# Optimization experiments

Hardware: AMD Instinct MI355X
Metric: run time of the kernel (lower is better)

## Reference

```python
import jax, jax.numpy as jnp
import numpy as np

B, GNN_DIM, TR_DIM, F = 16384, 512, 768, 1024


def setup_inputs() -> dict:
    key = jax.random.key(0)
    ks = jax.random.split(key, 16)
    s = 0.02
    return {
        "gnn_features": jax.random.normal(ks[0], (B, GNN_DIM), jnp.float32),
        "transformer_features": jax.random.normal(ks[1], (B, TR_DIM), jnp.float32),
        # gnn_projector / transformer_projector (torch Linear: y = x @ W.T + b)
        "Wg": jax.random.normal(ks[2], (F, GNN_DIM), jnp.float32) * s,
        "bg": jnp.zeros((F,), jnp.float32),
        "Wt": jax.random.normal(ks[3], (F, TR_DIM), jnp.float32) * s,
        "bt": jnp.zeros((F,), jnp.float32),
        # MultiheadAttention value-projection slice of in_proj_weight and out_proj.
        # With seq_len==1 the softmax over a single key is identically 1, so the
        # attention output is exactly out_proj(v_proj(key)); Q/K projections do
        # not affect the output (their gradients are exactly zero).
        "Wv": jax.random.normal(ks[4], (F, F), jnp.float32) * s,
        "bv": jnp.zeros((F,), jnp.float32),
        "Wo": jax.random.normal(ks[5], (F, F), jnp.float32) * s,
        "bo": jnp.zeros((F,), jnp.float32),
        # fusion_layers: Linear(2F -> F), GELU, Dropout(eval: identity), Linear(F -> F)
        "W1": jax.random.normal(ks[6], (F, 2 * F), jnp.float32) * s,
        "b1": jnp.zeros((F,), jnp.float32),
        "W2": jax.random.normal(ks[7], (F, F), jnp.float32) * s,
        "b2": jnp.zeros((F,), jnp.float32),
    }


def reference(gnn_features, transformer_features, Wg, bg, Wt, bt, Wv, bv, Wo, bo, W1, b1, W2, b2):
    # projections to fusion space  [B, F]
    gnn_proj = gnn_features @ Wg.T + bg
    tr_proj = transformer_features @ Wt.T + bt
    # degenerate single-token cross-attention: softmax over 1 key == 1, so
    # attn(q, k, v=k) = out_proj(v_proj(k)) regardless of the query.
    gnn_attended = (tr_proj @ Wv.T + bv) @ Wo.T + bo   # attention(gnn_seq, tr_seq, tr_seq)
    tr_attended = (gnn_proj @ Wv.T + bv) @ Wo.T + bo   # attention(tr_seq, gnn_seq, gnn_seq)
    combined = jnp.concatenate([gnn_attended, tr_attended], axis=-1)  # [B, 2F]
    h = jax.nn.gelu(combined @ W1.T + b1, approximate=False)          # exact GELU (torch default)
    fused = h @ W2.T + b2
    return fused + gnn_proj + tr_proj
```

## Files before the change

kernel.cpp:

```cpp
#include <hip/hip_runtime.h>
#include <cmath>

#define GAS __attribute__((address_space(1)))
#define LAS __attribute__((address_space(3)))

typedef __bf16 bf16x8 __attribute__((ext_vector_type(8)));
typedef float f32x4 __attribute__((ext_vector_type(4)));
typedef float f32x16 __attribute__((ext_vector_type(16)));

__device__ __forceinline__ void gload16(const void* g, void* l) {
    __builtin_amdgcn_global_load_lds((const GAS void*)g, (LAS void*)l, 16, 0, 0);
}

__global__ void k_prep(const float* __restrict__ gnn, const float* __restrict__ tr,
                       const float* __restrict__ Wo, const float* __restrict__ W1,
                       const float* __restrict__ W2, const float* __restrict__ Wg,
                       const float* __restrict__ Wt, const float* __restrict__ Wv,
                       const float* __restrict__ bv, const float* __restrict__ bo,
                       const float* __restrict__ bt, const float* __restrict__ bg,
                       __bf16* __restrict__ X, __bf16* __restrict__ W1ab,
                       __bf16* __restrict__ Wp, __bf16* __restrict__ Wv_b,
                       __bf16* __restrict__ WoT, __bf16* __restrict__ WgT,
                       __bf16* __restrict__ WtT,
                       float* __restrict__ b_att, float* __restrict__ vb_t,
                       float* __restrict__ vb_g) {
    __shared__ float t[32][33];
    int b = blockIdx.x;
    int tid = threadIdx.x;
    if (b < 12928) {
        const float* src; __bf16* dst; int sld, dld, base, c8;
        if (b < 4096)       { src=gnn;     sld=512;  dst=X+1024;         dld=2304; base=0;     c8=64; }
        else if (b < 10240) { src=tr;      sld=768;  dst=X+1536;         dld=2304; base=4096;  c8=96; }
        else if (b < 10752) { src=W1;      sld=2048; dst=W1ab;           dld=1024; base=10240; c8=128; }
        else if (b < 11264) { src=W1+1024; sld=2048; dst=W1ab+1024*1024; dld=1024; base=10752; c8=128; }
        else if (b < 11776) { src=W2;      sld=1024; dst=Wp;             dld=2304; base=11264; c8=128; }
        else if (b < 12032) { src=Wg;      sld=512;  dst=Wp+1024;        dld=2304; base=11776; c8=64; }
        else if (b < 12416) { src=Wt;      sld=768;  dst=Wp+1536;        dld=2304; base=12032; c8=96; }
        else                { src=Wv;      sld=1024; dst=Wv_b;           dld=1024; base=12416; c8=128; }
        int idx = (b - base) * 256 + tid;
        int r = idx / c8;
        int c = (idx - r * c8) << 3;
        const float4* s = reinterpret_cast<const float4*>(src + (long)r * sld + c);
        float4 x0 = s[0], x1 = s[1];
        bf16x8 v;
        v[0]=(__bf16)x0.x; v[1]=(__bf16)x0.y; v[2]=(__bf16)x0.z; v[3]=(__bf16)x0.w;
        v[4]=(__bf16)x1.x; v[5]=(__bf16)x1.y; v[6]=(__bf16)x1.z; v[7]=(__bf16)x1.w;
        *reinterpret_cast<bf16x8*>(dst + (long)r * dld + c) = v;
    } else if (b < 15232) {
        int bb = b - 12928;
        const float* src; __bf16* dst; int R, C, tile;
        if (bb < 1024)      { src=Wo; dst=WoT; R=1024; C=1024; tile=bb; }
        else if (bb < 1536) { src=Wg; dst=WgT; R=1024; C=512;  tile=bb-1024; }
        else                { src=Wt; dst=WtT; R=1024; C=768;  tile=bb-1536; }
        int tx_n = C >> 5;
        int c0 = (tile % tx_n) << 5, r0 = (tile / tx_n) << 5;
        int tx = tid & 31, ty = tid >> 5;
        #pragma unroll
        for (int i = 0; i < 32; i += 8)
            t[ty + i][tx] = src[(long)(r0 + ty + i) * C + c0 + tx];
        __syncthreads();
        #pragma unroll
        for (int i = 0; i < 32; i += 8)
            dst[(long)(c0 + ty + i) * R + r0 + tx] = (__bf16)t[tx][ty + i];
    } else {
        int bb = b - 15232;
        const float* mat; const float* vec; float* dst; int i; bool addbo = false;
        if (bb < 1024)      { mat = Wo; vec = bv; dst = b_att; i = bb;        addbo = true; }
        else if (bb < 2048) { mat = Wv; vec = bt; dst = vb_t;  i = bb - 1024; }
        else                { mat = Wv; vec = bg; dst = vb_g;  i = bb - 2048; }
        float s = 0.f;
        for (int k = tid; k < 1024; k += 256) s += mat[(long)i * 1024 + k] * vec[k];
        float* red = &t[0][0];
        red[tid] = s;
        __syncthreads();
        for (int off = 128; off > 0; off >>= 1) {
            if (tid < off) red[tid] += red[tid + off];
            __syncthreads();
        }
        if (tid == 0) dst[i] = red[0] + (addbo ? bo[i] : 0.f);
    }
}

__global__ void k_bias_z2(const float* __restrict__ W1, const float* __restrict__ b_att,
                          const float* __restrict__ b1, const __bf16* __restrict__ U12,
                          const float* __restrict__ vb_t, const float* __restrict__ vb_g,
                          const float* __restrict__ bt, const float* __restrict__ bg,
                          const float* __restrict__ b2,
                          float* __restrict__ bz2, float* __restrict__ b_out) {
    int i = blockIdx.x;
    float s = 0.f;
    for (int k = threadIdx.x; k < 1024; k += 256) {
        s += (W1[(long)i * 2048 + k] + W1[(long)i * 2048 + 1024 + k]) * b_att[k];
        s += (float)U12[(long)i * 1024 + k] * vb_t[k];
        s += (float)U12[(long)(i + 1024) * 1024 + k] * vb_g[k];
    }
    __shared__ float red[256];
    red[threadIdx.x] = s;
    __syncthreads();
    for (int off = 128; off > 0; off >>= 1) {
        if (threadIdx.x < off) red[threadIdx.x] += red[threadIdx.x + off];
        __syncthreads();
    }
    if (threadIdx.x == 0) {
        bz2[i] = red[0] + b1[i];
        b_out[i] = b2[i] + bg[i] + bt[i];
    }
}

template <int MODE>
__device__ __forceinline__ void gemm128_body(
    char* lds,
    const __bf16* __restrict__ A, int lda,
    const __bf16* __restrict__ B, int ldb,
    void* __restrict__ Cv, int ldc,
    int K, int n_tiles, int bid) {
    const int tid = threadIdx.x;
    const int lane = tid & 63;
    const int wave = tid >> 6;
    const int wm = wave >> 1;
    const int wn = wave & 1;

    const int bn = bid % n_tiles;
    const int bm = bid / n_tiles;
    const int m0 = bm * 128, n0 = bn * 128;

    const int rowS = ((tid >> 6) << 4) + (tid & 15);
    const int colS = ((tid >> 4) & 3) << 3;
    const __bf16* Ag = A + (long)(m0 + rowS) * lda + colS;
    const __bf16* Bg = B + (long)(n0 + rowS) * ldb + colS;
    const long lda64 = (long)64 * lda;
    const long ldb64 = (long)64 * ldb;
    const int tid16 = tid * 16;
    const int l16 = lane * 16;
    const int fr = lane & 15;

    f32x4 acc[4][4] = {};
    const int nk = K >> 5;

    auto stage = [&](int buf, int kt) {
        const long ko = (long)kt * 32;
        gload16(Ag + ko,         lds + buf * 8192 + tid16);
        gload16(Ag + ko + lda64, lds + buf * 8192 + 4096 + tid16);
        gload16(Bg + ko,         lds + 16384 + buf * 8192 + tid16);
        gload16(Bg + ko + ldb64, lds + 16384 + buf * 8192 + 4096 + tid16);
    };

    stage(0, 0);
    for (int kt = 0; kt < nk; ++kt) {
        const int buf = kt & 1;
        __syncthreads();
        if (kt + 1 < nk) stage(buf ^ 1, kt + 1);
        const char* a_ = lds + buf * 8192 + (wm * 4) * 1024;
        const char* b_ = lds + 16384 + buf * 8192 + (wn * 4) * 1024;
        bf16x8 af[4], bfr[4];
        #pragma unroll
        for (int m = 0; m < 4; ++m) af[m] = *(const bf16x8*)(a_ + m * 1024 + l16);
        #pragma unroll
        for (int n = 0; n < 4; ++n) bfr[n] = *(const bf16x8*)(b_ + n * 1024 + l16);
        __builtin_amdgcn_s_setprio(1);
        #pragma unroll
        for (int m = 0; m < 4; ++m)
            #pragma unroll
            for (int n = 0; n < 4; ++n)
                acc[m][n] = __builtin_amdgcn_mfma_f32_16x16x32_bf16(af[m], bfr[n], acc[m][n], 0, 0, 0);
        __builtin_amdgcn_s_setprio(0);
    }
    __syncthreads();

    char* scr = lds + wave * 4352;
    const int r0q = (lane >> 4) << 2;
    #pragma unroll
    for (int mq = 0; mq < 4; ++mq) {
        #pragma unroll
        for (int n_ = 0; n_ < 4; ++n_) {
            #pragma unroll
            for (int r = 0; r < 4; ++r) {
                float v = acc[mq][n_][r];
                *(float*)(scr + (r0q + r) * 272 + (n_ * 16 + fr) * 4) = v;
            }
        }
        asm volatile("s_waitcnt lgkmcnt(0)" ::: "memory");
        if (MODE == 2) {
            #pragma unroll
            for (int rep = 0; rep < 4; ++rep) {
                int row = rep * 4 + (lane >> 4);
                f32x4 val = *(const f32x4*)(scr + row * 272 + (lane & 15) * 16);
                long grow = (long)(m0 + wm * 64 + mq * 16 + row);
                *(f32x4*)&((float*)Cv)[grow * ldc + n0 + wn * 64 + (lane & 15) * 4] = val;
            }
        } else {
            #pragma unroll
            for (int rep = 0; rep < 2; ++rep) {
                int row = rep * 8 + (lane >> 3);
                f32x4 v0 = *(const f32x4*)(scr + row * 272 + (lane & 7) * 32);
                f32x4 v1 = *(const f32x4*)(scr + row * 272 + (lane & 7) * 32 + 16);
                bf16x8 o;
                o[0] = (__bf16)v0[0]; o[1] = (__bf16)v0[1]; o[2] = (__bf16)v0[2]; o[3] = (__bf16)v0[3];
                o[4] = (__bf16)v1[0]; o[5] = (__bf16)v1[1]; o[6] = (__bf16)v1[2]; o[7] = (__bf16)v1[3];
                long grow = (long)(m0 + wm * 64 + mq * 16 + row);
                *(bf16x8*)&((__bf16*)Cv)[grow * ldc + n0 + wn * 64 + (lane & 7) * 8] = o;
            }
        }
        asm volatile("s_waitcnt lgkmcnt(0)" ::: "memory");
    }
}

__global__ __launch_bounds__(256, 4) void k_gemmL1(
    const __bf16* __restrict__ W1ab, const __bf16* __restrict__ WoT,
    const __bf16* __restrict__ WtT, const __bf16* __restrict__ WgT,
    const __bf16* __restrict__ Wv_b, __bf16* __restrict__ U12,
    __bf16* __restrict__ VtT, __bf16* __restrict__ VgT) {
    __shared__ char lds[32768];
    int b = blockIdx.x;
    if (b < 128)      gemm128_body<0>(lds, W1ab, 1024, WoT, 1024, U12, 1024, 1024, 8, b);
    else if (b < 176) gemm128_body<0>(lds, WtT, 1024, Wv_b, 1024, VtT, 1024, 1024, 8, b - 128);
    else              gemm128_body<0>(lds, WgT, 1024, Wv_b, 1024, VgT, 1024, 1024, 8, b - 176);
}

__global__ __launch_bounds__(256, 4) void k_gemmL2(
    const __bf16* __restrict__ U12, const __bf16* __restrict__ VtT,
    const __bf16* __restrict__ VgT, __bf16* __restrict__ M1) {
    __shared__ char lds[32768];
    int b = blockIdx.x;
    if (b < 48) gemm128_body<0>(lds, U12, 1024, VtT, 1024, M1 + 512, 1280, 1024, 6, b);
    else        gemm128_body<0>(lds, U12 + 1024 * 1024, 1024, VgT, 1024, M1, 1280, 1024, 4, b - 48);
}

template <int MODE>
__device__ __forceinline__ void gemm8_body(
    const __bf16* __restrict__ A, int lda,
    const __bf16* __restrict__ B, int ldb,
    void* __restrict__ Cv, int ldc,
    const float* __restrict__ bias,
    int K, int n_tiles) {
    __shared__ char lds[131072];

    const int tid = threadIdx.x;
    const int lane = tid & 63;
    const int wave = tid >> 6;
    const int wm = wave >> 2;
    const int wn = wave & 3;

    int bid = blockIdx.x;
    const int nwg = gridDim.x;
    if ((nwg & 7) == 0) bid = (bid & 7) * (nwg >> 3) + (bid >> 3);
    const int bn = bid % n_tiles;
    const int bm = bid / n_tiles;
    const int m0 = bm * 256, n0 = bn * 256;

    const int rowA = ((tid >> 7) << 4) + (tid & 15);
    const int colA = (((tid >> 6) & 1) << 5) + (((tid >> 4) & 3) << 3);
    const int rowB = ((tid >> 6) << 4) + (tid & 15);
    const int colB = (((tid >> 4) & 3) << 3);
    const __bf16* Ag = A + (long)(m0 + rowA) * lda + colA;
    const __bf16* Bg = B + (long)(n0 + rowB) * ldb + colB;
    const int tid16 = tid * 16;

    const int laneA = ((lane >> 4) & 1) * 2048 + (lane >> 5) * 256 + (lane & 15) * 16;
    const int laneB = ((lane >> 4) & 1) * 1024 + (lane >> 5) * 256 + (lane & 15) * 16;
    const int bnh = wn >> 1;
    const int bno = (wn & 1) * 4096;

    f32x16 acc[4][2] = {};
    bf16x8 af[2][2];
    bf16x8 bfr[2][2][2];

    const int nk = K >> 6;
    const int NI = nk >> 1;

#define STAGE_A(PAR, KT, MH, QH) \
    gload16(Ag + (long)(KT) * 64 + (long)((MH) * 128 + (QH) * 64) * lda, \
            lds + (PAR) * 32768 + (MH) * 16384 + (QH) * 8192 + tid16)
#define STAGE_B(PAR, KT, NH, KK) \
    gload16(Bg + (long)(KT) * 64 + (KK) * 32 + (long)((NH) * 128) * ldb, \
            lds + 65536 + (PAR) * 32768 + (NH) * 16384 + (KK) * 8192 + tid16)
#define VMC6 asm volatile("s_waitcnt vmcnt(6)" ::: "memory")
#define VMC0 asm volatile("s_waitcnt vmcnt(0)" ::: "memory")
#define BAR  __builtin_amdgcn_s_barrier()
#define LGKM0 asm volatile("s_waitcnt lgkmcnt(0)" ::: "memory")
#define RD_A32(PAR, QH, KK) { \
        const char* a_ = lds + (PAR) * 32768 + wm * 16384 + (QH) * 8192 + (KK) * 1024; \
        _Pragma("unroll") \
        for (int fm_ = 0; fm_ < 2; ++fm_) { \
            _Pragma("unroll") \
            for (int h_ = 0; h_ < 2; ++h_) \
                af[fm_][h_] = *(const bf16x8*)(a_ + fm_ * 4096 + h_ * 512 + laneA); } }
#define RD_B32(KK, PAR) { \
        const char* b_ = lds + 65536 + (PAR) * 32768 + bnh * 16384 + (KK) * 8192 + bno; \
        _Pragma("unroll") \
        for (int fn_ = 0; fn_ < 2; ++fn_) { \
            _Pragma("unroll") \
            for (int h_ = 0; h_ < 2; ++h_) \
                bfr[KK][h_][fn_] = *(const bf16x8*)(b_ + fn_ * 2048 + h_ * 512 + laneB); } }
#define MFMA8(QH, KK) { \
        __builtin_amdgcn_s_setprio(1); \
        _Pragma("unroll") \
        for (int h_ = 0; h_ < 2; ++h_) { \
            _Pragma("unroll") \
            for (int fm_ = 0; fm_ < 2; ++fm_) { \
                _Pragma("unroll") \
                for (int fn_ = 0; fn_ < 2; ++fn_) \
                    acc[(QH) * 2 + fm_][fn_] = __builtin_amdgcn_mfma_f32_32x32x16_bf16( \
                        af[fm_][h_], bfr[KK][h_][fn_], acc[(QH) * 2 + fm_][fn_], 0, 0, 0); } } \
        __builtin_amdgcn_s_setprio(0); }

    STAGE_A(0, 0, 0, 0); STAGE_A(0, 0, 1, 0);
    STAGE_B(0, 0, 0, 0); STAGE_B(0, 0, 1, 0);
    STAGE_B(0, 0, 0, 1); STAGE_B(0, 0, 1, 1);
    STAGE_A(0, 0, 0, 1); STAGE_A(0, 0, 1, 1);
    STAGE_A(1, 1, 0, 0); STAGE_A(1, 1, 1, 0);
    STAGE_B(1, 1, 0, 0); STAGE_B(1, 1, 1, 0);
    STAGE_B(1, 1, 0, 1); STAGE_B(1, 1, 1, 1);
    VMC6;
    BAR;

    for (int I = 0; I < NI; ++I) {
        const int t = 2 * I;
        const bool nl = (I + 1 < NI);
        RD_B32(0, 0); RD_A32(0, 0, 0);
        STAGE_A(1, t + 1, 0, 1); STAGE_A(1, t + 1, 1, 1);
        BAR; LGKM0; MFMA8(0, 0); BAR;
        RD_B32(1, 0); RD_A32(0, 0, 1);
        if (nl) { STAGE_B(0, t + 2, 0, 0); STAGE_B(0, t + 2, 1, 0); }
        BAR; LGKM0; MFMA8(0, 1); BAR;
        RD_A32(0, 1, 0);
        if (nl) { STAGE_A(0, t + 2, 0, 0); STAGE_A(0, t + 2, 1, 0); }
        BAR; LGKM0; MFMA8(1, 0); BAR;
        RD_A32(0, 1, 1);
        if (nl) { STAGE_B(0, t + 2, 0, 1); STAGE_B(0, t + 2, 1, 1); VMC6; } else { VMC0; }
        BAR; LGKM0; MFMA8(1, 1); BAR;
        RD_B32(0, 1); RD_A32(1, 0, 0);
        if (nl) { STAGE_A(0, t + 2, 0, 1); STAGE_A(0, t + 2, 1, 1); }
        BAR; LGKM0; MFMA8(0, 0); BAR;
        RD_B32(1, 1); RD_A32(1, 0, 1);
        if (nl) { STAGE_B(1, t + 3, 0, 0); STAGE_B(1, t + 3, 1, 0); }
        BAR; LGKM0; MFMA8(0, 1); BAR;
        RD_A32(1, 1, 0);
        if (nl) { STAGE_A(1, t + 3, 0, 0); STAGE_A(1, t + 3, 1, 0); }
        BAR; LGKM0; MFMA8(1, 0); BAR;
        RD_A32(1, 1, 1);
        if (nl) { STAGE_B(1, t + 3, 0, 1); STAGE_B(1, t + 3, 1, 1); VMC6; }
        BAR; LGKM0; MFMA8(1, 1); BAR;
    }
#undef MFMA8
#undef RD_B32
#undef RD_A32
#undef LGKM0
#undef BAR
#undef VMC0
#undef VMC6
#undef STAGE_B
#undef STAGE_A

    char* scr = lds + wave * 16384;
    const int col32 = lane & 31;
    const int rb5 = (lane >> 5) << 2;
    float bval[2];
    bval[0] = bias ? bias[n0 + wn * 64 + col32] : 0.0f;
    bval[1] = bias ? bias[n0 + wn * 64 + 32 + col32] : 0.0f;

    #pragma unroll
    for (int FM = 0; FM < 4; ++FM) {
        #pragma unroll
        for (int fn_ = 0; fn_ < 2; ++fn_) {
            #pragma unroll
            for (int rg = 0; rg < 16; ++rg) {
                float v = acc[FM][fn_][rg] + bval[fn_];
                if (MODE == 1) {
                    float u = v * (0.7978845608f + 0.0356774081f * v * v);
                    float e = __expf(-2.0f * fabsf(u));
                    float th = (1.0f - e) / (1.0f + e);
                    th = copysignf(th, u);
                    v = 0.5f * v * (1.0f + th);
                }
                int srow = (rg & 3) + ((rg >> 2) << 3) + rb5;
                *(float*)(scr + srow * 272 + (fn_ * 32 + col32) * 4) = v;
            }
        }
        asm volatile("s_waitcnt lgkmcnt(0)" ::: "memory");
        if (MODE == 2) {
            #pragma unroll
            for (int rep = 0; rep < 8; ++rep) {
                int row = rep * 4 + (lane >> 4);
                f32x4 val = *(const f32x4*)(scr + row * 272 + (lane & 15) * 16);
                long grow = (long)(m0 + wm * 128 + FM * 32 + row);
                *(f32x4*)&((float*)Cv)[grow * ldc + n0 + wn * 64 + (lane & 15) * 4] = val;
            }
        } else {
            #pragma unroll
            for (int rep = 0; rep < 4; ++rep) {
                int row = rep * 8 + (lane >> 3);
                f32x4 v0 = *(const f32x4*)(scr + row * 272 + (lane & 7) * 32);
                f32x4 v1 = *(const f32x4*)(scr + row * 272 + (lane & 7) * 32 + 16);
                bf16x8 o;
                o[0] = (__bf16)v0[0]; o[1] = (__bf16)v0[1]; o[2] = (__bf16)v0[2]; o[3] = (__bf16)v0[3];
                o[4] = (__bf16)v1[0]; o[5] = (__bf16)v1[1]; o[6] = (__bf16)v1[2]; o[7] = (__bf16)v1[3];
                long grow = (long)(m0 + wm * 128 + FM * 32 + row);
                *(bf16x8*)&((__bf16*)Cv)[grow * ldc + n0 + wn * 64 + (lane & 7) * 8] = o;
            }
        }
        asm volatile("s_waitcnt lgkmcnt(0)" ::: "memory");
    }
}

__global__ __launch_bounds__(512, 2) void k_g256_gelu(
    const __bf16* __restrict__ A, int lda, const __bf16* __restrict__ B, int ldb,
    void* __restrict__ Cv, int ldc, const float* __restrict__ bias, int K, int n_tiles) {
    gemm8_body<1>(A, lda, B, ldb, Cv, ldc, bias, K, n_tiles);
}
__global__ __launch_bounds__(512, 2) void k_g256_out(
    const __bf16* __restrict__ A, int lda, const __bf16* __restrict__ B, int ldb,
    void* __restrict__ Cv, int ldc, const float* __restrict__ bias, int K, int n_tiles) {
    gemm8_body<2>(A, lda, B, ldb, Cv, ldc, bias, K, n_tiles);
}

extern "C" void kernel_launch(void* const* d_in, const int* in_sizes, int n_in,
                              void* d_out, int out_size, void* d_ws, size_t ws_size,
                              hipStream_t stream) {
    constexpr int Bsz = 16384, F = 1024, GD = 512, TD = 768;
    constexpr int XLD = F + GD + TD;

    const float* gnn = (const float*)d_in[0];
    const float* tr  = (const float*)d_in[1];
    const float* Wg  = (const float*)d_in[2];
    const float* bg  = (const float*)d_in[3];
    const float* Wt  = (const float*)d_in[4];
    const float* bt  = (const float*)d_in[5];
    const float* Wv  = (const float*)d_in[6];
    const float* bv  = (const float*)d_in[7];
    const float* Wo  = (const float*)d_in[8];
    const float* bo  = (const float*)d_in[9];
    const float* W1  = (const float*)d_in[10];
    const float* b1  = (const float*)d_in[11];
    const float* W2  = (const float*)d_in[12];
    const float* b2  = (const float*)d_in[13];
    float* out = (float*)d_out;

    char* w = (char*)d_ws;
    auto alloc = [&](size_t bytes) {
        char* p = w;
        w += (bytes + 255) & ~(size_t)255;
        return p;
    };
    __bf16* X    = (__bf16*)alloc((size_t)Bsz * XLD * 2);
    __bf16* M1   = (__bf16*)alloc((size_t)F * (GD + TD) * 2);
    __bf16* Wp   = (__bf16*)alloc((size_t)F * XLD * 2);
    __bf16* W1ab = (__bf16*)alloc((size_t)2 * F * F * 2);
    __bf16* Wv_b = (__bf16*)alloc((size_t)F * F * 2);
    __bf16* WoT  = (__bf16*)alloc((size_t)F * F * 2);
    __bf16* WgT  = (__bf16*)alloc((size_t)GD * F * 2);
    __bf16* WtT  = (__bf16*)alloc((size_t)TD * F * 2);
    __bf16* U12  = (__bf16*)alloc((size_t)2 * F * F * 2);
    __bf16* VtT  = (__bf16*)alloc((size_t)TD * F * 2);
    __bf16* VgT  = (__bf16*)alloc((size_t)GD * F * 2);
    float* b_att = (float*)alloc(F * 4);
    float* vb_t  = (float*)alloc(F * 4);
    float* vb_g  = (float*)alloc(F * 4);
    float* bz2   = (float*)alloc(F * 4);
    float* b_out = (float*)alloc(F * 4);
    if ((size_t)(w - (char*)d_ws) > ws_size) return;

    dim3 b256(256);

    k_prep<<<dim3(18304), b256, 0, stream>>>(gnn, tr, Wo, W1, W2, Wg, Wt, Wv,
                                             bv, bo, bt, bg,
                                             X, W1ab, Wp, Wv_b, WoT, WgT, WtT,
                                             b_att, vb_t, vb_g);

    k_gemmL1<<<dim3(208), b256, 0, stream>>>(W1ab, WoT, WtT, WgT, Wv_b, U12, VtT, VgT);

    k_bias_z2<<<dim3(F), b256, 0, stream>>>(W1, b_att, b1, U12, vb_t, vb_g, bt, bg, b2,
                                            bz2, b_out);

    k_gemmL2<<<dim3(80), b256, 0, stream>>>(U12, VtT, VgT, M1);

    k_g256_gelu<<<dim3((Bsz / 256) * (F / 256)), dim3(512), 0, stream>>>(
        X + F, XLD, M1, GD + TD, X, XLD, bz2, GD + TD, F / 256);

    k_g256_out<<<dim3((Bsz / 256) * (F / 256)), dim3(512), 0, stream>>>(
        X, XLD, Wp, XLD, out, F, b_out, XLD, F / 256);
}
```

Before: 221.6 us.

## Fuse GELU and output GEMMs with per-row-block flags; merge bias kernel into L2

Merges the two large 256x256 GEMM kernels into one persistent-style kernel. Each workgroup first computes its GELU tile, then signals a per-row-block counter and spin-waits until all four N-tiles of that row block are written before running the output GEMM. The bias-reduction kernel is folded into the L2 GEMM launch as extra blocks. This removes launch gaps and tail effects between kernels. The cost is a flag memset and spin-wait synchronisation, which relies on all 256 workgroups being co-resident (2 per CU) to avoid deadlock.

```diff
diff --git a/kernel.cpp b/kernel.cpp
--- a/kernel.cpp
+++ b/kernel.cpp
@@ -81,32 +81,6 @@
     }
 }
 
-__global__ void k_bias_z2(const float* __restrict__ W1, const float* __restrict__ b_att,
-                          const float* __restrict__ b1, const __bf16* __restrict__ U12,
-                          const float* __restrict__ vb_t, const float* __restrict__ vb_g,
-                          const float* __restrict__ bt, const float* __restrict__ bg,
-                          const float* __restrict__ b2,
-                          float* __restrict__ bz2, float* __restrict__ b_out) {
-    int i = blockIdx.x;
-    float s = 0.f;
-    for (int k = threadIdx.x; k < 1024; k += 256) {
-        s += (W1[(long)i * 2048 + k] + W1[(long)i * 2048 + 1024 + k]) * b_att[k];
-        s += (float)U12[(long)i * 1024 + k] * vb_t[k];
-        s += (float)U12[(long)(i + 1024) * 1024 + k] * vb_g[k];
-    }
-    __shared__ float red[256];
-    red[threadIdx.x] = s;
-    __syncthreads();
-    for (int off = 128; off > 0; off >>= 1) {
-        if (threadIdx.x < off) red[threadIdx.x] += red[threadIdx.x + off];
-        __syncthreads();
-    }
-    if (threadIdx.x == 0) {
-        bz2[i] = red[0] + b1[i];
-        b_out[i] = b2[i] + bg[i] + bt[i];
-    }
-}
-
 template <int MODE>
 __device__ __forceinline__ void gemm128_body(
     char* lds,
@@ -180,26 +154,16 @@
             }
         }
         asm volatile("s_waitcnt lgkmcnt(0)" ::: "memory");
-        if (MODE == 2) {
-            #pragma unroll
-            for (int rep = 0; rep < 4; ++rep) {
-                int row = rep * 4 + (lane >> 4);
-                f32x4 val = *(const f32x4*)(scr + row * 272 + (lane & 15) * 16);
-                long grow = (long)(m0 + wm * 64 + mq * 16 + row);
-                *(f32x4*)&((float*)Cv)[grow * ldc + n0 + wn * 64 + (lane & 15) * 4] = val;
-            }
-        } else {
-            #pragma unroll
-            for (int rep = 0; rep < 2; ++rep) {
-                int row = rep * 8 + (lane >> 3);
-                f32x4 v0 = *(const f32x4*)(scr + row * 272 + (lane & 7) * 32);
-                f32x4 v1 = *(const f32x4*)(scr + row * 272 + (lane & 7) * 32 + 16);
-                bf16x8 o;
-                o[0] = (__bf16)v0[0]; o[1] = (__bf16)v0[1]; o[2] = (__bf16)v0[2]; o[3] = (__bf16)v0[3];
-                o[4] = (__bf16)v1[0]; o[5] = (__bf16)v1[1]; o[6] = (__bf16)v1[2]; o[7] = (__bf16)v1[3];
-                long grow = (long)(m0 + wm * 64 + mq * 16 + row);
-                *(bf16x8*)&((__bf16*)Cv)[grow * ldc + n0 + wn * 64 + (lane & 7) * 8] = o;
-            }
+        #pragma unroll
+        for (int rep = 0; rep < 2; ++rep) {
+            int row = rep * 8 + (lane >> 3);
+            f32x4 v0 = *(const f32x4*)(scr + row * 272 + (lane & 7) * 32);
+            f32x4 v1 = *(const f32x4*)(scr + row * 272 + (lane & 7) * 32 + 16);
+            bf16x8 o;
+            o[0] = (__bf16)v0[0]; o[1] = (__bf16)v0[1]; o[2] = (__bf16)v0[2]; o[3] = (__bf16)v0[3];
+            o[4] = (__bf16)v1[0]; o[5] = (__bf16)v1[1]; o[6] = (__bf16)v1[2]; o[7] = (__bf16)v1[3];
+            long grow = (long)(m0 + wm * 64 + mq * 16 + row);
+            *(bf16x8*)&((__bf16*)Cv)[grow * ldc + n0 + wn * 64 + (lane & 7) * 8] = o;
         }
         asm volatile("s_waitcnt lgkmcnt(0)" ::: "memory");
     }
@@ -219,31 +183,53 @@
 
 __global__ __launch_bounds__(256, 4) void k_gemmL2(
     const __bf16* __restrict__ U12, const __bf16* __restrict__ VtT,
-    const __bf16* __restrict__ VgT, __bf16* __restrict__ M1) {
+    const __bf16* __restrict__ VgT, __bf16* __restrict__ M1,
+    const float* __restrict__ W1, const float* __restrict__ b_att,
+    const float* __restrict__ b1, const float* __restrict__ vb_t,
+    const float* __restrict__ vb_g, const float* __restrict__ bt,
+    const float* __restrict__ bg, const float* __restrict__ b2,
+    float* __restrict__ bz2, float* __restrict__ b_out) {
     __shared__ char lds[32768];
     int b = blockIdx.x;
-    if (b < 48) gemm128_body<0>(lds, U12, 1024, VtT, 1024, M1 + 512, 1280, 1024, 6, b);
-    else        gemm128_body<0>(lds, U12 + 1024 * 1024, 1024, VgT, 1024, M1, 1280, 1024, 4, b - 48);
+    if (b < 48)      gemm128_body<0>(lds, U12, 1024, VtT, 1024, M1 + 512, 1280, 1024, 6, b);
+    else if (b < 80) gemm128_body<0>(lds, U12 + 1024 * 1024, 1024, VgT, 1024, M1, 1280, 1024, 4, b - 48);
+    else {
+        int i = b - 80;
+        int tid = threadIdx.x;
+        float s = 0.f;
+        for (int k = tid; k < 1024; k += 256) {
+            s += (W1[(long)i * 2048 + k] + W1[(long)i * 2048 + 1024 + k]) * b_att[k];
+            s += (float)U12[(long)i * 1024 + k] * vb_t[k];
+            s += (float)U12[(long)(i + 1024) * 1024 + k] * vb_g[k];
+        }
+        float* red = (float*)lds;
+        red[tid] = s;
+        __syncthreads();
+        for (int off = 128; off > 0; off >>= 1) {
+            if (tid < off) red[tid] += red[tid + off];
+            __syncthreads();
+        }
+        if (tid == 0) {
+            bz2[i] = red[0] + b1[i];
+            b_out[i] = b2[i] + bg[i] + bt[i];
+        }
+    }
 }
 
 template <int MODE>
 __device__ __forceinline__ void gemm8_body(
+    char* lds,
     const __bf16* __restrict__ A, int lda,
     const __bf16* __restrict__ B, int ldb,
     void* __restrict__ Cv, int ldc,
     const float* __restrict__ bias,
-    int K, int n_tiles) {
-    __shared__ char lds[131072];
-
+    int K, int n_tiles, int bid) {
     const int tid = threadIdx.x;
     const int lane = tid & 63;
     const int wave = tid >> 6;
     const int wm = wave >> 2;
     const int wn = wave & 3;
 
-    int bid = blockIdx.x;
-    const int nwg = gridDim.x;
-    if ((nwg & 7) == 0) bid = (bid & 7) * (nwg >> 3) + (bid >> 3);
     const int bn = bid % n_tiles;
     const int bm = bid / n_tiles;
     const int m0 = bm * 256, n0 = bn * 256;
@@ -403,15 +389,31 @@
     }
 }
 
-__global__ __launch_bounds__(512, 2) void k_g256_gelu(
-    const __bf16* __restrict__ A, int lda, const __bf16* __restrict__ B, int ldb,
-    void* __restrict__ Cv, int ldc, const float* __restrict__ bias, int K, int n_tiles) {
-    gemm8_body<1>(A, lda, B, ldb, Cv, ldc, bias, K, n_tiles);
-}
-__global__ __launch_bounds__(512, 2) void k_g256_out(
-    const __bf16* __restrict__ A, int lda, const __bf16* __restrict__ B, int ldb,
-    void* __restrict__ Cv, int ldc, const float* __restrict__ bias, int K, int n_tiles) {
-    gemm8_body<2>(A, lda, B, ldb, Cv, ldc, bias, K, n_tiles);
+__global__ __launch_bounds__(512, 2) void k_fused(
+    __bf16* __restrict__ X, const __bf16* __restrict__ M1,
+    const __bf16* __restrict__ Wp, const float* __restrict__ bz2,
+    const float* __restrict__ b_out, float* __restrict__ out,
+    unsigned* __restrict__ flags) {
+    __shared__ char lds[131072];
+    int bid = blockIdx.x;
+    const int nwg = gridDim.x;
+    bid = (bid & 7) * (nwg >> 3) + (bid >> 3);
+    const int bm = bid >> 2;
+
+    gemm8_body<1>(lds, X + 1024, 2304, M1, 1280, X, 2304, bz2, 1280, 4, bid);
+
+    __threadfence();
+    __syncthreads();
+    if (threadIdx.x == 0)
+        __hip_atomic_fetch_add(&flags[bm], 1u, __ATOMIC_RELEASE, __HIP_MEMORY_SCOPE_AGENT);
+    if (threadIdx.x == 0) {
+        while (__hip_atomic_load(&flags[bm], __ATOMIC_ACQUIRE, __HIP_MEMORY_SCOPE_AGENT) < 4u)
+            __builtin_amdgcn_s_sleep(8);
+    }
+    __syncthreads();
+    __threadfence();
+
+    gemm8_body<2>(lds, X, 2304, Wp, 2304, out, 1024, b_out, 2304, 4, bid);
 }
 
 extern "C" void kernel_launch(void* const* d_in, const int* in_sizes, int n_in,
@@ -458,9 +460,12 @@
     float* vb_g  = (float*)alloc(F * 4);
     float* bz2   = (float*)alloc(F * 4);
     float* b_out = (float*)alloc(F * 4);
+    unsigned* flags = (unsigned*)alloc(64 * 4);
     if ((size_t)(w - (char*)d_ws) > ws_size) return;
 
     dim3 b256(256);
+
+    hipMemsetAsync(flags, 0, 64 * 4, stream);
 
     k_prep<<<dim3(18304), b256, 0, stream>>>(gnn, tr, Wo, W1, W2, Wg, Wt, Wv,
                                              bv, bo, bt, bg,
@@ -469,14 +474,9 @@
 
     k_gemmL1<<<dim3(208), b256, 0, stream>>>(W1ab, WoT, WtT, WgT, Wv_b, U12, VtT, VgT);
 
-    k_bias_z2<<<dim3(F), b256, 0, stream>>>(W1, b_att, b1, U12, vb_t, vb_g, bt, bg, b2,
-                                            bz2, b_out);
-
-    k_gemmL2<<<dim3(80), b256, 0, stream>>>(U12, VtT, VgT, M1);
-
-    k_g256_gelu<<<dim3((Bsz / 256) * (F / 256)), dim3(512), 0, stream>>>(
-        X + F, XLD, M1, GD + TD, X, XLD, bz2, GD + TD, F / 256);
-
-    k_g256_out<<<dim3((Bsz / 256) * (F / 256)), dim3(512), 0, stream>>>(
-        X, XLD, Wp, XLD, out, F, b_out, XLD, F / 256);
-}
+    k_gemmL2<<<dim3(1104), b256, 0, stream>>>(U12, VtT, VgT, M1,
+                                              W1, b_att, b1, vb_t, vb_g, bt, bg, b2,
+                                              bz2, b_out);
+
+    k_fused<<<dim3(256), dim3(512), 0, stream>>>(X, M1, Wp, bz2, b_out, out, flags);
+}
```

Result: slower. 309.3 us (+39.5%).
